# Kernel optimization log

Measured on AMD Instinct MI355X. Metric: run time of the kernel, lower is better.

## Reference

```python
import jax, jax.numpy as jnp
import numpy as np
from jax import lax

RATIO = 0.25
RADIUS = 0.2
NSAMPLE = 32


def _fps(xyz, S):
    # xyz: [B, N, 3] -> indices [B, S] via farthest point sampling (start at 0)
    B, N, _ = xyz.shape

    def body(carry, _):
        dist, farthest = carry  # dist [B,N], farthest [B]
        centroid = jnp.take_along_axis(xyz, farthest[:, None, None], axis=1)  # [B,1,3]
        d = jnp.sum((xyz - centroid) ** 2, axis=-1)  # [B,N]
        dist = jnp.minimum(dist, d)
        nxt = jnp.argmax(dist, axis=-1).astype(jnp.int32)
        return (dist, nxt), farthest

    init = (jnp.full((B, N), 1e10, dtype=xyz.dtype), jnp.zeros((B,), jnp.int32))
    _, idx = lax.scan(body, init, None, length=S)  # [S, B]
    return idx.T  # [B, S]


def _ball_query(radius, nsample, xyz, new_xyz):
    # xyz: [B,N,3], new_xyz: [B,S,3] -> neighbor indices [B,S,nsample]
    B, N, _ = xyz.shape
    sqr = jnp.sum((new_xyz[:, :, None, :] - xyz[:, None, :, :]) ** 2, axis=-1)  # [B,S,N]
    arange = jnp.arange(N, dtype=jnp.int32)[None, None, :]
    idx = jnp.where(sqr <= radius * radius, arange, N)  # out-of-ball -> sentinel N
    idx = jnp.sort(idx, axis=-1)[:, :, :nsample]  # first nsample in-ball points
    first = idx[:, :, :1]
    idx = jnp.where(idx == N, first, idx)  # pad with first valid neighbor
    return idx


def reference(xyz, features, w1, b1, w2, b2, w3, b3):
    # xyz: [B,N,3]; features unused in the non-group_all branch (faithful to source).
    B, N, _ = xyz.shape
    S = int(RATIO * N)

    fps_idx = _fps(xyz, S)  # [B,S]
    new_xyz = jnp.take_along_axis(xyz, fps_idx[:, :, None], axis=1)  # [B,S,3]

    nbr_idx = _ball_query(RADIUS, NSAMPLE, xyz, new_xyz)  # [B,S,K]
    b_idx = jnp.arange(B, dtype=jnp.int32)[:, None, None]
    grouped = xyz[b_idx, nbr_idx]  # [B,S,K,3]
    rel = grouped - new_xyz[:, :, None, :]  # center-relative coords

    # new_points.permute(0,3,2,1): [B,S,K,C] -> [B,C,K,S]; shared 1x1 conv MLP + ReLU
    x = rel.transpose(0, 3, 2, 1)  # [B,3,K,S]
    x = jax.nn.relu(jnp.einsum('bcks,oc->boks', x, w1) + b1[None, :, None, None])
    x = jax.nn.relu(jnp.einsum('bcks,oc->boks', x, w2) + b2[None, :, None, None])
    x = jax.nn.relu(jnp.einsum('bcks,oc->boks', x, w3) + b3[None, :, None, None])

    new_points = jnp.max(x, axis=2)  # max over nsample -> [B,128,S]
    return new_xyz.transpose(0, 2, 1), new_points  # [B,3,S], [B,128,S]


def setup_inputs() -> dict:
    key = jax.random.key(0)
    ks = jax.random.split(key, 8)
    B, N = 8, 8192
    xyz = jax.random.uniform(ks[0], (B, N, 3), dtype=jnp.float32)
    features = jax.random.normal(ks[1], (B, 64, N), dtype=jnp.float32)
    w1 = jax.random.normal(ks[2], (64, 3), dtype=jnp.float32) * (1.0 / np.sqrt(3))
    b1 = jnp.zeros((64,), jnp.float32)
    w2 = jax.random.normal(ks[3], (64, 64), dtype=jnp.float32) * (1.0 / np.sqrt(64))
    b2 = jnp.zeros((64,), jnp.float32)
    w3 = jax.random.normal(ks[4], (128, 64), dtype=jnp.float32) * (1.0 / np.sqrt(64))
    b3 = jnp.zeros((128,), jnp.float32)
    return {"xyz": xyz, "features": features, "w1": w1, "b1": b1,
            "w2": w2, "b2": b2, "w3": w3, "b3": b3}
```

## Files before the change

### kernel.cpp

```cpp
#include <hip/hip_runtime.h>
#include <cstdint>
#include <cstddef>

#define BB 8
#define NN 8192
#define SS 2048
#define KNB 32

__device__ __forceinline__ float sqdist_exact(float ax, float ay, float az,
                                              float bx, float by, float bz) {
#pragma clang fp contract(off)
    float dx = ax - bx;
    float dy = ay - by;
    float dz = az - bz;
    return (dx * dx + dy * dy) + dz * dz;
}

template <int CTRL>
__device__ __forceinline__ float dpp_fmax_step(float x) {
    int t = __builtin_amdgcn_update_dpp(__float_as_int(-1.0f), __float_as_int(x),
                                        CTRL, 0xf, 0xf, false);
    return fmaxf(x, __int_as_float(t));
}
template <int CTRL>
__device__ __forceinline__ int dpp_imin_step(int x) {
    int t = __builtin_amdgcn_update_dpp(0x7fffffff, x, CTRL, 0xf, 0xf, false);
    return min(x, t);
}
template <int CTRL>
__device__ __forceinline__ unsigned long long dpp_u64max_step(unsigned long long k) {
    int lo = __builtin_amdgcn_update_dpp(0, (int)(unsigned)(k & 0xffffffffu),
                                         CTRL, 0xf, 0xf, false);
    int hi = __builtin_amdgcn_update_dpp(0, (int)(unsigned)(k >> 32),
                                         CTRL, 0xf, 0xf, false);
    unsigned long long o = ((unsigned long long)(unsigned)hi << 32) | (unsigned)lo;
    return (o > k) ? o : k;
}
#define ROW_SHR1 0x111
#define ROW_SHR2 0x112
#define ROW_SHR4 0x114
#define ROW_SHR8 0x118
#define ROW_BC15 0x142
#define ROW_BC31 0x143

__device__ __forceinline__ void wave_minmax(float x, float& lo, float& hi) {
    float a = x, b = x;
#pragma unroll
    for (int off = 1; off < 64; off <<= 1) {
        a = fminf(a, __shfl_xor(a, off));
        b = fmaxf(b, __shfl_xor(b, off));
    }
    lo = a;
    hi = b;
}

__global__ void prep_kernel(const float* __restrict__ w1, const float* __restrict__ w2,
                            const float* __restrict__ w3, float* __restrict__ w1T,
                            float* __restrict__ w2T, float* __restrict__ w3T) {
    for (int i = threadIdx.x; i < 192; i += 256) {
        int oc = i / 3, c = i % 3;
        w1T[c * 64 + oc] = w1[i];
    }
    for (int i = threadIdx.x; i < 4096; i += 256) {
        int oc = i >> 6, j = i & 63;
        w2T[j * 64 + oc] = w2[i];
    }
    for (int i = threadIdx.x; i < 8192; i += 256) {
        int oc = i >> 6, j = i & 63;
        w3T[j * 128 + oc] = w3[i];
    }
}

__device__ __forceinline__ int part3(int v) {
    return (v & 1) | ((v & 2) << 2) | ((v & 4) << 4);
}

#define PT_LIST(X) X(0) X(1) X(2) X(3) X(4) X(5) X(6) X(7) \
                   X(8) X(9) X(10) X(11) X(12) X(13) X(14) X(15)

__global__ __attribute__((amdgpu_flat_work_group_size(512, 512),
                          amdgpu_waves_per_eu(2, 2)))
void fps_kernel(const float* __restrict__ xyz_all,
                float4* __restrict__ wsSorted,
                float4* __restrict__ wsCtr,
                float* __restrict__ out0) {
    const int b = blockIdx.x;
    const float* xyz = xyz_all + (size_t)b * NN * 3;
    float4* sorted = wsSorted + (size_t)b * NN;
    float4* ctr = wsCtr + (size_t)b * SS;
    float* o0 = out0 + (size_t)b * 3 * SS;

    __shared__ float xLds[NN];
    __shared__ float yLds[NN];
    __shared__ float zLds[NN];
    __shared__ float4 ctrLds[SS];
    __shared__ int cellCnt[512];
    __shared__ int cellBase[512];
    __shared__ unsigned long long red[2][8];

    const int tid = threadIdx.x;
    const int wid = tid >> 6;
    const int lane = tid & 63;

    cellCnt[tid] = 0;
    __syncthreads();
    int cellReg[16];
#pragma unroll
    for (int j = 0; j < 16; ++j) {
        int p = tid + j * 512;
        float x = xyz[p * 3 + 0], y = xyz[p * 3 + 1], z = xyz[p * 3 + 2];
        xLds[p] = x; yLds[p] = y; zLds[p] = z;
        int qx = min(7, (int)(x * 8.0f));
        int qy = min(7, (int)(y * 8.0f));
        int qz = min(7, (int)(z * 8.0f));
        cellReg[j] = part3(qx) | (part3(qy) << 1) | (part3(qz) << 2);
        atomicAdd(&cellCnt[cellReg[j]], 1);
    }
    __syncthreads();
    int myCnt = cellCnt[tid];
    for (int off = 1; off < 512; off <<= 1) {
        int v = (tid >= off) ? cellCnt[tid - off] : 0;
        __syncthreads();
        cellCnt[tid] += v;
        __syncthreads();
    }
    cellBase[tid] = cellCnt[tid] - myCnt;
    __syncthreads();
#pragma unroll
    for (int j = 0; j < 16; ++j) {
        int p = tid + j * 512;
        float x = xLds[p], y = yLds[p], z = zLds[p];
        int pos = atomicAdd(&cellBase[cellReg[j]], 1);
        sorted[pos] = make_float4(x, y, z, __int_as_float(p));
    }
    __threadfence();
    __syncthreads();

#define DECL_PT(i)                                      \
    float px##i, py##i, pz##i, dist##i;                 \
    int od##i;                                          \
    {                                                   \
        float4 v = sorted[(wid * 16 + i) * 64 + lane];  \
        px##i = v.x; py##i = v.y; pz##i = v.z;          \
        od##i = __float_as_int(v.w);                    \
        dist##i = 1e10f;                                \
    }
    PT_LIST(DECL_PT)

    float bbxlo = 0.f, bbxhi = 0.f, bbylo = 0.f, bbyhi = 0.f,
          bbzlo = 0.f, bbzhi = 0.f;
#define BRICK_BB(i)                                               \
    {                                                             \
        float xl, xh, yl, yh, zl, zh;                             \
        wave_minmax(px##i, xl, xh);                               \
        wave_minmax(py##i, yl, yh);                               \
        wave_minmax(pz##i, zl, zh);                               \
        if (lane == i) {                                          \
            bbxlo = xl; bbxhi = xh;                               \
            bbylo = yl; bbyhi = yh;                               \
            bbzlo = zl; bbzhi = zh;                               \
        }                                                         \
    }
    PT_LIST(BRICK_BB)

    float cx = xLds[0], cy = yLds[0], cz = zLds[0];
    if (tid == 0) ctrLds[0] = make_float4(cx, cy, cz, 0.0f);

    unsigned long long waveKey =
        ((unsigned long long)__float_as_uint(1e10f) << 32) | 0xFFFFFFFFull;
    float wave_bv = 1e10f;

    for (int s = 1; s < SS; ++s) {
        const int par = s & 1;
        float ddx = fmaxf(fmaxf(bbxlo - cx, cx - bbxhi), 0.0f);
        float ddy = fmaxf(fmaxf(bbylo - cy, cy - bbyhi), 0.0f);
        float ddz = fmaxf(fmaxf(bbzlo - cz, cz - bbzhi), 0.0f);
        float lb2 = (ddx * ddx + ddy * ddy) + ddz * ddz;
        bool act = (lane < 16) && (lb2 * 0.999f < wave_bv);
        unsigned mask = (unsigned)__builtin_amdgcn_readfirstlane(
            (int)(unsigned)__ballot(act));
        if (mask) {
#define UPD_BR(i)                                                     \
    if (mask & (1u << i)) {                                           \
        float d = sqdist_exact(px##i, py##i, pz##i, cx, cy, cz);      \
        dist##i = fminf(dist##i, d);                                  \
    }
            PT_LIST(UPD_BR)
            float nbv = -1.0f;
#define NBV_PT(i) nbv = fmaxf(nbv, dist##i);
            PT_LIST(NBV_PT)
            float m = nbv;
            m = dpp_fmax_step<ROW_SHR1>(m);
            m = dpp_fmax_step<ROW_SHR2>(m);
            m = dpp_fmax_step<ROW_SHR4>(m);
            m = dpp_fmax_step<ROW_SHR8>(m);
            m = dpp_fmax_step<ROW_BC15>(m);
            m = dpp_fmax_step<ROW_BC31>(m);
            float wv = __int_as_float(__builtin_amdgcn_readlane(__float_as_int(m), 63));
            int cand = 0x7fffffff;
#define IDX_PT(i) cand = (dist##i == wv) ? min(cand, od##i) : cand;
            PT_LIST(IDX_PT)
            cand = dpp_imin_step<ROW_SHR1>(cand);
            cand = dpp_imin_step<ROW_SHR2>(cand);
            cand = dpp_imin_step<ROW_SHR4>(cand);
            cand = dpp_imin_step<ROW_SHR8>(cand);
            cand = dpp_imin_step<ROW_BC15>(cand);
            cand = dpp_imin_step<ROW_BC31>(cand);
            int wiw = __builtin_amdgcn_readlane(cand, 63);
            waveKey = ((unsigned long long)__float_as_uint(wv) << 32) |
                      (unsigned)(~(unsigned)wiw);
            wave_bv = wv;
        }
        if (lane == 0) red[par][wid] = waveKey;
        __syncthreads();
        unsigned long long k = red[par][lane & 7];
        k = dpp_u64max_step<ROW_SHR1>(k);
        k = dpp_u64max_step<ROW_SHR2>(k);
        k = dpp_u64max_step<ROW_SHR4>(k);
        unsigned blo = (unsigned)__builtin_amdgcn_readlane(
            (int)(unsigned)(k & 0xffffffffu), 7);
        int wiu = (int)(~blo);
        cx = xLds[wiu];
        cy = yLds[wiu];
        cz = zLds[wiu];
        if (tid == 0) ctrLds[s] = make_float4(cx, cy, cz, 0.0f);
    }

    __syncthreads();
    for (int s = tid; s < SS; s += 512) {
        float4 c = ctrLds[s];
        o0[s] = c.x;
        o0[SS + s] = c.y;
        o0[2 * SS + s] = c.z;
        ctr[s] = c;
    }
}

__global__ __launch_bounds__(128) void bqmlp_kernel(const float* __restrict__ xyz_all,
                                                    const float4* __restrict__ wsCtr,
                                                    const float* __restrict__ w1T,
                                                    const float* __restrict__ b1,
                                                    const float* __restrict__ w2T,
                                                    const float* __restrict__ b2,
                                                    const float* __restrict__ w3T,
                                                    const float* __restrict__ b3,
                                                    float* __restrict__ out1) {
    const int b = blockIdx.x >> 10;
    const int s0 = (blockIdx.x & 1023) * 2;
    const float* xyz = xyz_all + (size_t)b * NN * 3;

    __shared__ float relF[2 * KNB * 3];
    __shared__ float hT[64 * 64];

    const int tid = threadIdx.x;
    const int cb = __builtin_amdgcn_readfirstlane(tid >> 6);
    const int l = tid & 63;

    {
        float4 cc = wsCtr[(size_t)b * SS + s0 + cb];
        float ccx = cc.x, ccy = cc.y, ccz = cc.z;
        const float R2 = (float)(0.2 * 0.2);
        int total = 0;
        float fx = 0.f, fy = 0.f, fz = 0.f;
        bool have = false;
        for (int chunk = 0; chunk < 128 && total < KNB; ++chunk) {
            int p = chunk * 64 + l;
            float x = xyz[p * 3 + 0], y = xyz[p * 3 + 1], z = xyz[p * 3 + 2];
            float d = sqdist_exact(ccx, ccy, ccz, x, y, z);
            bool hit = (d <= R2);
            unsigned long long mask = __ballot(hit);
            int cnt = __popcll(mask);
            if (cnt) {
                int pos = total + __popcll(mask & ((1ull << l) - 1ull));
                float rx = x - ccx, ry = y - ccy, rz = z - ccz;
                if (hit && pos < KNB) {
                    relF[(cb * KNB + pos) * 3 + 0] = rx;
                    relF[(cb * KNB + pos) * 3 + 1] = ry;
                    relF[(cb * KNB + pos) * 3 + 2] = rz;
                }
                if (hit && pos == 0) { fx = rx; fy = ry; fz = rz; have = true; }
                total += cnt;
            }
        }
        unsigned long long hm = __ballot(have);
        if (total < KNB) {
            int src = __ffsll((long long)hm) - 1;
            float gx = __shfl(fx, src), gy = __shfl(fy, src), gz = __shfl(fz, src);
            if (l >= total && l < KNB) {
                relF[(cb * KNB + l) * 3 + 0] = gx;
                relF[(cb * KNB + l) * 3 + 1] = gy;
                relF[(cb * KNB + l) * 3 + 2] = gz;
            }
        }
    }
    __syncthreads();

    const int r = l;

    {
        float rx = relF[r * 3 + 0], ry = relF[r * 3 + 1], rz = relF[r * 3 + 2];
#pragma unroll
        for (int i = 0; i < 32; ++i) {
            int ch = cb * 32 + i;
            float h = b1[ch];
            h = fmaf(rx, w1T[0 * 64 + ch], h);
            h = fmaf(ry, w1T[1 * 64 + ch], h);
            h = fmaf(rz, w1T[2 * 64 + ch], h);
            hT[ch * 64 + r] = fmaxf(h, 0.0f);
        }
    }
    __syncthreads();

    {
        float acc[32];
#pragma unroll
        for (int i = 0; i < 32; ++i) acc[i] = b2[cb * 32 + i];
#pragma unroll 4
        for (int j = 0; j < 64; ++j) {
            float a = hT[j * 64 + r];
            const float* wrow = w2T + j * 64 + cb * 32;
#pragma unroll
            for (int i = 0; i < 32; ++i) acc[i] = fmaf(a, wrow[i], acc[i]);
        }
        __syncthreads();
#pragma unroll
        for (int i = 0; i < 32; ++i) hT[(cb * 32 + i) * 64 + r] = fmaxf(acc[i], 0.0f);
    }
    __syncthreads();

    {
        float acc[64];
#pragma unroll
        for (int i = 0; i < 64; ++i) acc[i] = b3[cb * 64 + i];
#pragma unroll 2
        for (int j = 0; j < 64; ++j) {
            float a = hT[j * 64 + r];
            const float* wrow = w3T + j * 128 + cb * 64;
#pragma unroll
            for (int i = 0; i < 64; ++i) acc[i] = fmaf(a, wrow[i], acc[i]);
        }
#pragma unroll
        for (int i = 0; i < 64; ++i) {
            float v = fmaxf(acc[i], 0.0f);
            v = fmaxf(v, __shfl_xor(v, 1));
            v = fmaxf(v, __shfl_xor(v, 2));
            v = fmaxf(v, __shfl_xor(v, 4));
            v = fmaxf(v, __shfl_xor(v, 8));
            v = fmaxf(v, __shfl_xor(v, 16));
            acc[i] = v;
        }
        if ((l & 31) == 0) {
            int sA = s0 + (l >> 5);
            float* op = out1 + ((size_t)b * 128 + cb * 64) * SS + sA;
#pragma unroll
            for (int i = 0; i < 64; ++i) op[(size_t)i * SS] = acc[i];
        }
    }
}

extern "C" void kernel_launch(void* const* d_in, const int* in_sizes, int n_in,
                              void* d_out, int out_size, void* d_ws, size_t ws_size,
                              hipStream_t stream) {
    (void)in_sizes; (void)n_in; (void)out_size; (void)ws_size;
    const float* xyz = (const float*)d_in[0];
    const float* w1 = (const float*)d_in[2];
    const float* b1 = (const float*)d_in[3];
    const float* w2 = (const float*)d_in[4];
    const float* b2 = (const float*)d_in[5];
    const float* w3 = (const float*)d_in[6];
    const float* b3 = (const float*)d_in[7];
    float* out = (float*)d_out;

    float4* wsCtr = (float4*)d_ws;
    float4* wsSorted = wsCtr + BB * SS;
    float* w1T = (float*)(wsSorted + BB * NN);
    float* w2T = w1T + 192;
    float* w3T = w2T + 4096;

    prep_kernel<<<1, 256, 0, stream>>>(w1, w2, w3, w1T, w2T, w3T);
    fps_kernel<<<BB, 512, 0, stream>>>(xyz, wsSorted, wsCtr, out);
    bqmlp_kernel<<<BB * (SS / 2), 128, 0, stream>>>(xyz, wsCtr, w1T, b1, w2T, b2,
                                                    w3T, b3, out + BB * 3 * SS);
}
```

Baseline: 1.998 ms.

## Cache per-brick argmax keys and re-reduce only updated bricks in FPS

The FPS inner loop now keeps a cached packed (distance, index) max key per brick in lanes 0-15. Only bricks whose distances were updated recompute their key with a 64-bit DPP reduction. The wave-level max then reduces just those 16 cached keys, and the per-lane pruning bound uses each brick's own cached max instead of the wave max. This tighter per-brick bound should skip more updates and avoids the full max-then-index double reduction. The cost is a separate 64-bit reduction for every active brick, which may be expensive when many bricks are active.

```diff
diff --git a/kernel.cpp b/kernel.cpp
--- a/kernel.cpp
+++ b/kernel.cpp
@@ -16,17 +16,6 @@
     return (dx * dx + dy * dy) + dz * dz;
 }
 
-template <int CTRL>
-__device__ __forceinline__ float dpp_fmax_step(float x) {
-    int t = __builtin_amdgcn_update_dpp(__float_as_int(-1.0f), __float_as_int(x),
-                                        CTRL, 0xf, 0xf, false);
-    return fmaxf(x, __int_as_float(t));
-}
-template <int CTRL>
-__device__ __forceinline__ int dpp_imin_step(int x) {
-    int t = __builtin_amdgcn_update_dpp(0x7fffffff, x, CTRL, 0xf, 0xf, false);
-    return min(x, t);
-}
 template <int CTRL>
 __device__ __forceinline__ unsigned long long dpp_u64max_step(unsigned long long k) {
     int lo = __builtin_amdgcn_update_dpp(0, (int)(unsigned)(k & 0xffffffffu),
@@ -166,17 +155,20 @@
     float cx = xLds[0], cy = yLds[0], cz = zLds[0];
     if (tid == 0) ctrLds[0] = make_float4(cx, cy, cz, 0.0f);
 
+    int bkeyLo = 0;
+    int bkeyHi = (lane < 16) ? (int)__float_as_uint(1e10f) : 0;
+
     unsigned long long waveKey =
         ((unsigned long long)__float_as_uint(1e10f) << 32) | 0xFFFFFFFFull;
-    float wave_bv = 1e10f;
 
     for (int s = 1; s < SS; ++s) {
         const int par = s & 1;
+        float bv = __int_as_float(bkeyHi);
         float ddx = fmaxf(fmaxf(bbxlo - cx, cx - bbxhi), 0.0f);
         float ddy = fmaxf(fmaxf(bbylo - cy, cy - bbyhi), 0.0f);
         float ddz = fmaxf(fmaxf(bbzlo - cz, cz - bbzhi), 0.0f);
         float lb2 = (ddx * ddx + ddy * ddy) + ddz * ddz;
-        bool act = (lane < 16) && (lb2 * 0.999f < wave_bv);
+        bool act = (lane < 16) && (lb2 * 0.999f < bv);
         unsigned mask = (unsigned)__builtin_amdgcn_readfirstlane(
             (int)(unsigned)__ballot(act));
         if (mask) {
@@ -186,30 +178,34 @@
         dist##i = fminf(dist##i, d);                                  \
     }
             PT_LIST(UPD_BR)
-            float nbv = -1.0f;
-#define NBV_PT(i) nbv = fmaxf(nbv, dist##i);
-            PT_LIST(NBV_PT)
-            float m = nbv;
-            m = dpp_fmax_step<ROW_SHR1>(m);
-            m = dpp_fmax_step<ROW_SHR2>(m);
-            m = dpp_fmax_step<ROW_SHR4>(m);
-            m = dpp_fmax_step<ROW_SHR8>(m);
-            m = dpp_fmax_step<ROW_BC15>(m);
-            m = dpp_fmax_step<ROW_BC31>(m);
-            float wv = __int_as_float(__builtin_amdgcn_readlane(__float_as_int(m), 63));
-            int cand = 0x7fffffff;
-#define IDX_PT(i) cand = (dist##i == wv) ? min(cand, od##i) : cand;
-            PT_LIST(IDX_PT)
-            cand = dpp_imin_step<ROW_SHR1>(cand);
-            cand = dpp_imin_step<ROW_SHR2>(cand);
-            cand = dpp_imin_step<ROW_SHR4>(cand);
-            cand = dpp_imin_step<ROW_SHR8>(cand);
-            cand = dpp_imin_step<ROW_BC15>(cand);
-            cand = dpp_imin_step<ROW_BC31>(cand);
-            int wiw = __builtin_amdgcn_readlane(cand, 63);
-            waveKey = ((unsigned long long)__float_as_uint(wv) << 32) |
-                      (unsigned)(~(unsigned)wiw);
-            wave_bv = wv;
+#define REKEY_BR(i)                                                            \
+    if (mask & (1u << i)) {                                                    \
+        unsigned long long k =                                                 \
+            ((unsigned long long)__float_as_uint(dist##i) << 32) |             \
+            (unsigned)(~(unsigned)od##i);                                      \
+        k = dpp_u64max_step<ROW_SHR1>(k);                                      \
+        k = dpp_u64max_step<ROW_SHR2>(k);                                      \
+        k = dpp_u64max_step<ROW_SHR4>(k);                                      \
+        k = dpp_u64max_step<ROW_SHR8>(k);                                      \
+        k = dpp_u64max_step<ROW_BC15>(k);                                      \
+        k = dpp_u64max_step<ROW_BC31>(k);                                      \
+        int klo = __builtin_amdgcn_readlane((int)(unsigned)(k & 0xffffffffu), 63); \
+        int khi = __builtin_amdgcn_readlane((int)(unsigned)(k >> 32), 63);     \
+        bkeyLo = (lane == i) ? klo : bkeyLo;                                   \
+        bkeyHi = (lane == i) ? khi : bkeyHi;                                   \
+    }
+            PT_LIST(REKEY_BR)
+            unsigned long long wk =
+                ((unsigned long long)(unsigned)bkeyHi << 32) | (unsigned)bkeyLo;
+            wk = dpp_u64max_step<ROW_SHR1>(wk);
+            wk = dpp_u64max_step<ROW_SHR2>(wk);
+            wk = dpp_u64max_step<ROW_SHR4>(wk);
+            wk = dpp_u64max_step<ROW_SHR8>(wk);
+            unsigned wlo = (unsigned)__builtin_amdgcn_readlane(
+                (int)(unsigned)(wk & 0xffffffffu), 15);
+            unsigned whi = (unsigned)__builtin_amdgcn_readlane(
+                (int)(unsigned)(wk >> 32), 15);
+            waveKey = ((unsigned long long)whi << 32) | wlo;
         }
         if (lane == 0) red[par][wid] = waveKey;
         __syncthreads();
```

Result: slower. 3.786 ms (+89.4%).
